# Kernel optimization log

Hardware: AMD Instinct MI355X
Metric: run time of the kernel (lower is better)

## Reference

```python
import jax, jax.numpy as jnp
import numpy as np

BLOCK = 128          # quantization block size
F8_MAX = 448.0       # max representable magnitude of float8_e4m3fn


def setup_inputs() -> dict:
    key = jax.random.key(0)
    k1, k2, k3 = jax.random.split(key, 3)
    M, K, N = 8192, 4096, 4096
    Kb, Nb = K // BLOCK, N // BLOCK
    x = jax.random.normal(k1, (M, K), jnp.float32)
    # weight stored as fp8-representable values (simulated with f32 container)
    weight = jax.random.normal(k2, (N, K), jnp.float32)
    # per 128x128-block weight dequant scales (positive, small, like amax/448)
    weight_scale = jax.random.uniform(k3, (Nb, Kb), jnp.float32, 0.5, 1.5) * 0.01
    return {"x": x, "weight": weight, "weight_scale": weight_scale}


def _act_quant(x):
    """fp8_blockwise_act_quant: per-(row, 128-block) scale = amax/448, cast to e4m3."""
    M, K = x.shape
    Kb = K // BLOCK
    xb = x.reshape(M, Kb, BLOCK)
    amax = jnp.max(jnp.abs(xb), axis=-1, keepdims=True)            # [M, Kb, 1]
    scale = jnp.maximum(amax, 1e-12) / F8_MAX                      # [M, Kb, 1]
    xq = (xb / scale).astype(jnp.float8_e4m3fn).astype(jnp.float32)
    return xq, scale


def reference(x, weight, weight_scale):
    # ---- activation blockwise fp8 quant ----
    xq, x_scale = _act_quant(x)                                    # [M,Kb,B], [M,Kb,1]
    M, Kb, _ = xq.shape
    K = Kb * BLOCK
    x_deq = (xq * x_scale).reshape(M, K)                           # dequantized activations

    # ---- weight blockwise fp8 dequant (weight stored as fp8 values) ----
    N = weight.shape[0]
    Nb = N // BLOCK
    wq = weight.astype(jnp.float8_e4m3fn).astype(jnp.float32)      # fp8 storage
    w_deq = (wq.reshape(Nb, BLOCK, Kb, BLOCK)
             * weight_scale[:, None, :, None]).reshape(N, K)

    # ---- scaled GEMM: y = x_deq @ w_deq^T (bias is None) ----
    return x_deq @ w_deq.T                                         # [M, N]
```

## Files before the change

### kernel.cpp

```cpp
#include <hip/hip_runtime.h>


#define GLOBAL_AS __attribute__((address_space(1)))
#define LDS_AS    __attribute__((address_space(3)))

typedef int   v4i __attribute__((ext_vector_type(4)));
typedef int   v8i __attribute__((ext_vector_type(8)));
typedef float v4f __attribute__((ext_vector_type(4)));

constexpr int M  = 8192;
constexpr int K  = 4096;
constexpr int N  = 4096;
constexpr int KB = K / 128;
constexpr int NB = N / 128;

__device__ __forceinline__ void async16(const void* g, void* l) {
  __builtin_amdgcn_global_load_lds((const GLOBAL_AS void*)g, (LDS_AS void*)l, 16, 0, 0);
}

__global__ __launch_bounds__(256) void quant_x_kernel(
    const float* __restrict__ x, unsigned char* __restrict__ xq,
    float* __restrict__ xs_t ) {
  const int tid = threadIdx.x;
  const long long blk = (long long)blockIdx.x * 8 + (tid >> 5);
  const int l = tid & 31;
  const float4 v = ((const float4*)(x + blk * 128))[l];
  float ax = fmaxf(fmaxf(fabsf(v.x), fabsf(v.y)), fmaxf(fabsf(v.z), fabsf(v.w)));
#pragma unroll
  for (int s = 16; s >= 1; s >>= 1) ax = fmaxf(ax, __shfl_xor(ax, s, 32));
  const float scale = fmaxf(ax, 1e-12f) / 448.0f;
  int p = 0;
  p = __builtin_amdgcn_cvt_pk_fp8_f32(v.x / scale, v.y / scale, p, false);
  p = __builtin_amdgcn_cvt_pk_fp8_f32(v.z / scale, v.w / scale, p, true);
  ((int*)(xq + blk * 128))[l] = p;
  if (l == 0) {
    const int m  = (int)(blk >> 5);
    const int kb = (int)(blk & (KB - 1));
    xs_t[(long long)kb * M + m] = scale;
  }
}

__global__ __launch_bounds__(256) void quant_w_kernel(
    const float* __restrict__ w, unsigned char* __restrict__ wq) {
  const long long i = (long long)blockIdx.x * 256 + threadIdx.x;
  const float4 v = ((const float4*)w)[i];
  int p = 0;
  p = __builtin_amdgcn_cvt_pk_fp8_f32(v.x, v.y, p, false);
  p = __builtin_amdgcn_cvt_pk_fp8_f32(v.z, v.w, p, true);
  ((int*)wq)[i] = p;
}

__global__ __launch_bounds__(256, 2) void gemm_fp8_kernel(
    const unsigned char* __restrict__ xq, const unsigned char* __restrict__ wq,
    const float* __restrict__ xs_t ,
    const float* __restrict__ wscale ,
    float* __restrict__ out) {
  __shared__ unsigned char Asm[128 * 128];
  __shared__ unsigned char Bsm[128 * 128];
  __shared__ float Ssm[KB * 128];

  const int tid   = threadIdx.x;
  const int ntile = blockIdx.x;
  const int mtile = blockIdx.y;
  const int wave  = tid >> 6;
  const int lane  = tid & 63;
  const int wm = wave >> 1, wn = wave & 1;
  const int l15 = lane & 15, quad = lane >> 4;

  for (int i = tid; i < KB * 128; i += 256) {
    const int kb = i >> 7, r = i & 127;
    Ssm[i] = xs_t[(long long)kb * M + mtile * 128 + r] * wscale[ntile * KB + kb];
  }

  const int s_r8 = lane >> 3, s_ch = lane & 7;
  const unsigned char* pa[4];
  const unsigned char* pb[4];
#pragma unroll
  for (int t = 0; t < 4; ++t) {
    const int lrow = wave * 32 + t * 8 + s_r8;
    const int cc   = ((s_ch ^ s_r8) << 4);
    pa[t] = xq + (long long)(mtile * 128 + lrow) * K + cc;
    pb[t] = wq + (long long)(ntile * 128 + lrow) * K + cc;
  }
  const int lds_base = wave * 32 * 128;

  int aoff[4][2], boff[4][2], soff[4];
#pragma unroll
  for (int f = 0; f < 4; ++f) {
    const int m_loc = wm * 64 + f * 16 + l15;
    const int n_loc = wn * 64 + f * 16 + l15;
    aoff[f][0] = m_loc * 128 + (((quad * 2 + 0) ^ (m_loc & 7)) << 4);
    aoff[f][1] = m_loc * 128 + (((quad * 2 + 1) ^ (m_loc & 7)) << 4);
    boff[f][0] = n_loc * 128 + (((quad * 2 + 0) ^ (n_loc & 7)) << 4);
    boff[f][1] = n_loc * 128 + (((quad * 2 + 1) ^ (n_loc & 7)) << 4);
    soff[f] = wm * 64 + f * 16 + quad * 4;
  }

  v4f acc[4][4];
#pragma unroll
  for (int f = 0; f < 4; ++f)
#pragma unroll
    for (int g = 0; g < 4; ++g) acc[f][g] = (v4f){0.f, 0.f, 0.f, 0.f};

  for (int kb = 0; kb < KB; ++kb) {
    const int koff = kb * 128;
#pragma unroll
    for (int t = 0; t < 4; ++t) {
      async16(pa[t] + koff, Asm + lds_base + t * 1024);
      async16(pb[t] + koff, Bsm + lds_base + t * 1024);
    }
    __syncthreads();

    v8i a[4], b[4];
#pragma unroll
    for (int f = 0; f < 4; ++f) {
      v4i lo = *(const v4i*)(Asm + aoff[f][0]);
      v4i hi = *(const v4i*)(Asm + aoff[f][1]);
      a[f][0] = lo[0]; a[f][1] = lo[1]; a[f][2] = lo[2]; a[f][3] = lo[3];
      a[f][4] = hi[0]; a[f][5] = hi[1]; a[f][6] = hi[2]; a[f][7] = hi[3];
      v4i lo2 = *(const v4i*)(Bsm + boff[f][0]);
      v4i hi2 = *(const v4i*)(Bsm + boff[f][1]);
      b[f][0] = lo2[0]; b[f][1] = lo2[1]; b[f][2] = lo2[2]; b[f][3] = lo2[3];
      b[f][4] = hi2[0]; b[f][5] = hi2[1]; b[f][6] = hi2[2]; b[f][7] = hi2[3];
    }
    v4f sx[4];
#pragma unroll
    for (int f = 0; f < 4; ++f) sx[f] = *(const v4f*)(Ssm + kb * 128 + soff[f]);

#pragma unroll
    for (int f = 0; f < 4; ++f) {
#pragma unroll
      for (int g = 0; g < 4; ++g) {
        const v4f z = (v4f){0.f, 0.f, 0.f, 0.f};
        v4f p = __builtin_amdgcn_mfma_scale_f32_16x16x128_f8f6f4(
            a[f], b[g], z, 0, 0, 0, 0x7f7f7f7f, 0, 0x7f7f7f7f);
        acc[f][g] += sx[f] * p;
      }
    }
    __syncthreads();
  }

#pragma unroll
  for (int f = 0; f < 4; ++f) {
#pragma unroll
    for (int r = 0; r < 4; ++r) {
      const long long row = mtile * 128 + wm * 64 + f * 16 + quad * 4 + r;
      float* po = out + row * N + ntile * 128 + wn * 64 + l15;
#pragma unroll
      for (int g = 0; g < 4; ++g) po[g * 16] = acc[f][g][r];
    }
  }
}

extern "C" void kernel_launch(void* const* d_in, const int* in_sizes, int n_in,
                              void* d_out, int out_size, void* d_ws, size_t ws_size,
                              hipStream_t stream) {
  const float* x   = (const float*)d_in[0];
  const float* w   = (const float*)d_in[1];
  const float* wsc = (const float*)d_in[2];
  float* out = (float*)d_out;

  unsigned char* ws = (unsigned char*)d_ws;
  unsigned char* xq = ws;
  unsigned char* wq = ws + (size_t)M * K;
  float* xs_t = (float*)(ws + (size_t)M * K + (size_t)N * K);

  quant_x_kernel<<<M * KB / 8, 256, 0, stream>>>(x, xq, xs_t);
  quant_w_kernel<<<(N * (long long)K) / 1024, 256, 0, stream>>>(w, wq);
  gemm_fp8_kernel<<<dim3(N / 128, M / 128), 256, 0, stream>>>(xq, wq, xs_t, wsc, out);
}
```

Before: 435.3 us.

## Pre-swizzle fp8 operands into MFMA fragment layout and load directly to registers

The quant kernels now write the fp8 activations and weights in a tiled layout that matches the MFMA operand fragments, so each lane's 16-byte chunks are contiguous. The GEMM drops LDS staging for A and B and loads fragments straight from global memory into registers, double-buffered across k-blocks, which removes the per-iteration barriers. The cost is that each wave fetches its own operands with no sharing through LDS, so there is more global/L2 traffic and higher register pressure.

```diff
diff --git a/kernel.cpp b/kernel.cpp
--- a/kernel.cpp
+++ b/kernel.cpp
@@ -1,8 +1,5 @@
 #include <hip/hip_runtime.h>
 
-
-#define GLOBAL_AS __attribute__((address_space(1)))
-#define LDS_AS    __attribute__((address_space(3)))
 
 typedef int   v4i __attribute__((ext_vector_type(4)));
 typedef int   v8i __attribute__((ext_vector_type(8)));
@@ -14,40 +11,66 @@
 constexpr int KB = K / 128;
 constexpr int NB = N / 128;
 
-__device__ __forceinline__ void async16(const void* g, void* l) {
-  __builtin_amdgcn_global_load_lds((const GLOBAL_AS void*)g, (LDS_AS void*)l, 16, 0, 0);
-}
 
 __global__ __launch_bounds__(256) void quant_x_kernel(
     const float* __restrict__ x, unsigned char* __restrict__ xq,
     float* __restrict__ xs_t ) {
   const int tid = threadIdx.x;
-  const long long blk = (long long)blockIdx.x * 8 + (tid >> 5);
-  const int l = tid & 31;
-  const float4 v = ((const float4*)(x + blk * 128))[l];
-  float ax = fmaxf(fmaxf(fabsf(v.x), fabsf(v.y)), fmaxf(fabsf(v.z), fabsf(v.w)));
+  const long long blk = ((long long)blockIdx.x * 256 + tid) >> 3;
+  const int s = tid & 7;
+  const int m  = (int)(blk >> 5);
+  const int kb = (int)(blk & (KB - 1));
+
+  const float4* px = (const float4*)(x + blk * 128 + s * 16);
+  float4 v0 = px[0], v1 = px[1], v2 = px[2], v3 = px[3];
+
+  float ax = 0.f;
+#define AMAX4(v) ax = fmaxf(ax, fmaxf(fmaxf(fabsf(v.x), fabsf(v.y)), fmaxf(fabsf(v.z), fabsf(v.w))))
+  AMAX4(v0); AMAX4(v1); AMAX4(v2); AMAX4(v3);
+#undef AMAX4
 #pragma unroll
-  for (int s = 16; s >= 1; s >>= 1) ax = fmaxf(ax, __shfl_xor(ax, s, 32));
+  for (int d = 4; d >= 1; d >>= 1) ax = fmaxf(ax, __shfl_xor(ax, d, 8));
   const float scale = fmaxf(ax, 1e-12f) / 448.0f;
-  int p = 0;
-  p = __builtin_amdgcn_cvt_pk_fp8_f32(v.x / scale, v.y / scale, p, false);
-  p = __builtin_amdgcn_cvt_pk_fp8_f32(v.z / scale, v.w / scale, p, true);
-  ((int*)(xq + blk * 128))[l] = p;
-  if (l == 0) {
-    const int m  = (int)(blk >> 5);
-    const int kb = (int)(blk & (KB - 1));
-    xs_t[(long long)kb * M + m] = scale;
-  }
+
+  int p0 = 0, p1 = 0, p2 = 0, p3 = 0;
+  p0 = __builtin_amdgcn_cvt_pk_fp8_f32(v0.x / scale, v0.y / scale, p0, false);
+  p0 = __builtin_amdgcn_cvt_pk_fp8_f32(v0.z / scale, v0.w / scale, p0, true);
+  p1 = __builtin_amdgcn_cvt_pk_fp8_f32(v1.x / scale, v1.y / scale, p1, false);
+  p1 = __builtin_amdgcn_cvt_pk_fp8_f32(v1.z / scale, v1.w / scale, p1, true);
+  p2 = __builtin_amdgcn_cvt_pk_fp8_f32(v2.x / scale, v2.y / scale, p2, false);
+  p2 = __builtin_amdgcn_cvt_pk_fp8_f32(v2.z / scale, v2.w / scale, p2, true);
+  p3 = __builtin_amdgcn_cvt_pk_fp8_f32(v3.x / scale, v3.y / scale, p3, false);
+  p3 = __builtin_amdgcn_cvt_pk_fp8_f32(v3.z / scale, v3.w / scale, p3, true);
+
+  const int q = s >> 1, j = s & 1, rr = m & 15;
+  const long long base = ((long long)(m >> 4) * KB + kb) * 2048;
+  *(v4i*)(xq + base + j * 1024 + (q * 16 + rr) * 16) = (v4i){p0, p1, p2, p3};
+
+  if (s == 0) xs_t[(long long)kb * M + m] = scale;
 }
 
 __global__ __launch_bounds__(256) void quant_w_kernel(
     const float* __restrict__ w, unsigned char* __restrict__ wq) {
-  const long long i = (long long)blockIdx.x * 256 + threadIdx.x;
-  const float4 v = ((const float4*)w)[i];
-  int p = 0;
-  p = __builtin_amdgcn_cvt_pk_fp8_f32(v.x, v.y, p, false);
-  p = __builtin_amdgcn_cvt_pk_fp8_f32(v.z, v.w, p, true);
-  ((int*)wq)[i] = p;
+  const long long t = (long long)blockIdx.x * 256 + threadIdx.x;
+  const int grp = (int)(t >> 7);
+  const int idx = (int)(t & 127);
+  const int l = idx >> 1, j = idx & 1;
+  const int nf = grp >> 5, kb = grp & (KB - 1);
+  const int n = nf * 16 + (l & 15);
+  const int k = kb * 128 + (l >> 4) * 32 + j * 16;
+
+  const float4* pw = (const float4*)(w + (long long)n * K + k);
+  float4 v0 = pw[0], v1 = pw[1], v2 = pw[2], v3 = pw[3];
+  int p0 = 0, p1 = 0, p2 = 0, p3 = 0;
+  p0 = __builtin_amdgcn_cvt_pk_fp8_f32(v0.x, v0.y, p0, false);
+  p0 = __builtin_amdgcn_cvt_pk_fp8_f32(v0.z, v0.w, p0, true);
+  p1 = __builtin_amdgcn_cvt_pk_fp8_f32(v1.x, v1.y, p1, false);
+  p1 = __builtin_amdgcn_cvt_pk_fp8_f32(v1.z, v1.w, p1, true);
+  p2 = __builtin_amdgcn_cvt_pk_fp8_f32(v2.x, v2.y, p2, false);
+  p2 = __builtin_amdgcn_cvt_pk_fp8_f32(v2.z, v2.w, p2, true);
+  p3 = __builtin_amdgcn_cvt_pk_fp8_f32(v3.x, v3.y, p3, false);
+  p3 = __builtin_amdgcn_cvt_pk_fp8_f32(v3.z, v3.w, p3, true);
+  *(v4i*)(wq + (long long)grp * 2048 + j * 1024 + l * 16) = (v4i){p0, p1, p2, p3};
 }
 
 __global__ __launch_bounds__(256, 2) void gemm_fp8_kernel(
@@ -55,8 +78,6 @@
     const float* __restrict__ xs_t ,
     const float* __restrict__ wscale ,
     float* __restrict__ out) {
-  __shared__ unsigned char Asm[128 * 128];
-  __shared__ unsigned char Bsm[128 * 128];
   __shared__ float Ssm[KB * 128];
 
   const int tid   = threadIdx.x;
@@ -71,30 +92,16 @@
     const int kb = i >> 7, r = i & 127;
     Ssm[i] = xs_t[(long long)kb * M + mtile * 128 + r] * wscale[ntile * KB + kb];
   }
+  __syncthreads();
 
-  const int s_r8 = lane >> 3, s_ch = lane & 7;
-  const unsigned char* pa[4];
-  const unsigned char* pb[4];
+  const unsigned char* pa0 =
+      xq + ((long long)(mtile * 8 + wm * 4) * KB) * 2048 + lane * 16;
+  const unsigned char* pb0 =
+      wq + ((long long)(ntile * 8 + wn * 4) * KB) * 2048 + lane * 16;
+
+  int soff[4];
 #pragma unroll
-  for (int t = 0; t < 4; ++t) {
-    const int lrow = wave * 32 + t * 8 + s_r8;
-    const int cc   = ((s_ch ^ s_r8) << 4);
-    pa[t] = xq + (long long)(mtile * 128 + lrow) * K + cc;
-    pb[t] = wq + (long long)(ntile * 128 + lrow) * K + cc;
-  }
-  const int lds_base = wave * 32 * 128;
-
-  int aoff[4][2], boff[4][2], soff[4];
-#pragma unroll
-  for (int f = 0; f < 4; ++f) {
-    const int m_loc = wm * 64 + f * 16 + l15;
-    const int n_loc = wn * 64 + f * 16 + l15;
-    aoff[f][0] = m_loc * 128 + (((quad * 2 + 0) ^ (m_loc & 7)) << 4);
-    aoff[f][1] = m_loc * 128 + (((quad * 2 + 1) ^ (m_loc & 7)) << 4);
-    boff[f][0] = n_loc * 128 + (((quad * 2 + 0) ^ (n_loc & 7)) << 4);
-    boff[f][1] = n_loc * 128 + (((quad * 2 + 1) ^ (n_loc & 7)) << 4);
-    soff[f] = wm * 64 + f * 16 + quad * 4;
-  }
+  for (int f = 0; f < 4; ++f) soff[f] = wm * 64 + f * 16 + quad * 4;
 
   v4f acc[4][4];
 #pragma unroll
@@ -102,30 +109,42 @@
 #pragma unroll
     for (int g = 0; g < 4; ++g) acc[f][g] = (v4f){0.f, 0.f, 0.f, 0.f};
 
+  v4i aLo[2][4], aHi[2][4], bLo[2][4], bHi[2][4];
+
+#define LOADK(kb, buf)                                                  \
+  {                                                                     \
+    const unsigned char* pa = pa0 + (long long)(kb) * 2048;             \
+    const unsigned char* pb = pb0 + (long long)(kb) * 2048;             \
+    _Pragma("unroll") for (int f = 0; f < 4; ++f) {                     \
+      aLo[buf][f] = *(const v4i*)(pa + (long long)f * (KB * 2048));     \
+      aHi[buf][f] = *(const v4i*)(pa + (long long)f * (KB * 2048) + 1024); \
+      bLo[buf][f] = *(const v4i*)(pb + (long long)f * (KB * 2048));     \
+      bHi[buf][f] = *(const v4i*)(pb + (long long)f * (KB * 2048) + 1024); \
+    }                                                                   \
+  }
+
+  LOADK(0, 0);
+
   for (int kb = 0; kb < KB; ++kb) {
-    const int koff = kb * 128;
+    const int cur = kb & 1;
+    if (kb + 1 < KB) LOADK(kb + 1, cur ^ 1);
+
+    v4f sx[4];
 #pragma unroll
-    for (int t = 0; t < 4; ++t) {
-      async16(pa[t] + koff, Asm + lds_base + t * 1024);
-      async16(pb[t] + koff, Bsm + lds_base + t * 1024);
-    }
-    __syncthreads();
+    for (int f = 0; f < 4; ++f) sx[f] = *(const v4f*)(Ssm + kb * 128 + soff[f]);
 
     v8i a[4], b[4];
 #pragma unroll
     for (int f = 0; f < 4; ++f) {
-      v4i lo = *(const v4i*)(Asm + aoff[f][0]);
-      v4i hi = *(const v4i*)(Asm + aoff[f][1]);
-      a[f][0] = lo[0]; a[f][1] = lo[1]; a[f][2] = lo[2]; a[f][3] = lo[3];
-      a[f][4] = hi[0]; a[f][5] = hi[1]; a[f][6] = hi[2]; a[f][7] = hi[3];
-      v4i lo2 = *(const v4i*)(Bsm + boff[f][0]);
-      v4i hi2 = *(const v4i*)(Bsm + boff[f][1]);
-      b[f][0] = lo2[0]; b[f][1] = lo2[1]; b[f][2] = lo2[2]; b[f][3] = lo2[3];
-      b[f][4] = hi2[0]; b[f][5] = hi2[1]; b[f][6] = hi2[2]; b[f][7] = hi2[3];
+      a[f][0] = aLo[cur][f][0]; a[f][1] = aLo[cur][f][1];
+      a[f][2] = aLo[cur][f][2]; a[f][3] = aLo[cur][f][3];
+      a[f][4] = aHi[cur][f][0]; a[f][5] = aHi[cur][f][1];
+      a[f][6] = aHi[cur][f][2]; a[f][7] = aHi[cur][f][3];
+      b[f][0] = bLo[cur][f][0]; b[f][1] = bLo[cur][f][1];
+      b[f][2] = bLo[cur][f][2]; b[f][3] = bLo[cur][f][3];
+      b[f][4] = bHi[cur][f][0]; b[f][5] = bHi[cur][f][1];
+      b[f][6] = bHi[cur][f][2]; b[f][7] = bHi[cur][f][3];
     }
-    v4f sx[4];
-#pragma unroll
-    for (int f = 0; f < 4; ++f) sx[f] = *(const v4f*)(Ssm + kb * 128 + soff[f]);
 
 #pragma unroll
     for (int f = 0; f < 4; ++f) {
@@ -137,8 +156,8 @@
         acc[f][g] += sx[f] * p;
       }
     }
-    __syncthreads();
   }
+#undef LOADK
 
 #pragma unroll
   for (int f = 0; f < 4; ++f) {
@@ -165,7 +184,7 @@
   unsigned char* wq = ws + (size_t)M * K;
   float* xs_t = (float*)(ws + (size_t)M * K + (size_t)N * K);
 
-  quant_x_kernel<<<M * KB / 8, 256, 0, stream>>>(x, xq, xs_t);
-  quant_w_kernel<<<(N * (long long)K) / 1024, 256, 0, stream>>>(w, wq);
-  gemm_fp8_kernel<<<dim3(N / 128, M / 128), 256, 0, stream>>>(xq, wq, xs_t, wsc, out);
+  quant_x_kernel<<<(M * KB * 8) / 256, 256, 0, stream>>>(x, xq, xs_t);
+  quant_w_kernel<<<(int)(((long long)N * K / 16) / 256), 256, 0, stream>>>(w, wq);
+  gemm_fp8_kernel<<<dim3(NB, M / 128), 256, 0, stream>>>(xq, wq, xs_t, wsc, out);
 }
```

Result: slower. 968.7 us (+122.5%).
